# Optimization experiments

Hardware: AMD Instinct MI355X
Metric: run time of the kernel (lower is better)

## Reference

```python
import jax, jax.numpy as jnp
import numpy as np

NEG_INF = -9e15  # same masking constant as the torch module


def setup_inputs() -> dict:
    key = jax.random.key(0)
    k1, k2, k3 = jax.random.split(key, 3)
    B, S, F = 8, 2048, 128
    H, D = 4, 32  # n_heads, head_dim = out_features // n_heads
    features = jax.random.normal(k1, (B, S, F), dtype=jnp.float32)
    adj_matrix = jax.random.randint(k2, (B, S, S), 0, 2, dtype=jnp.int32)
    # Xavier-uniform-ish init for W [H, F, D]
    limit = float(np.sqrt(6.0 / (F + D)))
    W = jax.random.uniform(k3, (H, F, D), dtype=jnp.float32, minval=-limit, maxval=limit)
    return {"features": features, "adj_matrix": adj_matrix, "W": W}


def reference(features, adj_matrix, W):
    # features: [B, S, F], adj_matrix: [B, S, S] (>0 == edge), W: [H, F, D]
    D = W.shape[-1]
    Wh = jnp.einsum("bsf,hfd->bhsd", features, W)                 # [B, H, S, D]
    scores = jnp.einsum("bhsd,bhtd->bhst", Wh, Wh) / jnp.sqrt(jnp.float32(D))
    scores = jnp.where(adj_matrix[:, None, :, :] > 0, scores, NEG_INF)
    attn = jax.nn.softmax(scores, axis=-1)                         # [B, H, S, S]
    # dropout is identity at inference (training=False)
    h = jnp.einsum("bhst,bhtd->bhsd", attn, Wh)                    # [B, H, S, D]
    B, H, S, _ = h.shape
    # concat heads along feature dim, matching torch.cat(heads, dim=2)
    return jnp.transpose(h, (0, 2, 1, 3)).reshape(B, S, H * D)
```

## Files before the change

### kernel.cpp

```cpp
#include <hip/hip_runtime.h>
#include <hip/hip_bf16.h>
#include <stdint.h>


namespace {
constexpr int S = 2048;
constexpr int F = 128;
constexpr int H = 4;
constexpr int D = 32;

typedef __attribute__((ext_vector_type(4))) float f32x4;
typedef __attribute__((ext_vector_type(8))) short s16x8;
typedef __attribute__((ext_vector_type(4))) short s16x4;

__device__ __forceinline__ short f2bf(float f) {
  __hip_bfloat16 h = __float2bfloat16(f);
  short s; __builtin_memcpy(&s, &h, sizeof(s)); return s;
}
__device__ __forceinline__ float bf2f(short s) {
  __hip_bfloat16 h; __builtin_memcpy(&h, &s, sizeof(s));
  return __bfloat162float(h);
}
__device__ __forceinline__ f32x4 i4mask(int4 a) {
  f32x4 r;
  r[0] = a.x ? 1.0f : 0.0f; r[1] = a.y ? 1.0f : 0.0f;
  r[2] = a.z ? 1.0f : 0.0f; r[3] = a.w ? 1.0f : 0.0f;
  return r;
}

__global__ __launch_bounds__(256) void gat_proj(const float* __restrict__ feat,
                                                const float* __restrict__ W,
                                                short* __restrict__ Wh,
                                                short* __restrict__ WhT) {
  __shared__ __align__(16) short ftile[64][136];
  const int tid = threadIdx.x;
  const int w = tid >> 6;
  const int l = tid & 63;
  const int ln = l & 15, lg = l >> 4, g4 = (l >> 4) * 4;
  const int row0 = blockIdx.x * 64;
  const int b = row0 >> 11;
  const int sl0 = row0 & (S - 1);

#pragma unroll
  for (int i = 0; i < 4; ++i) {
    int c = i * 256 + tid;
    int r = c >> 4, c8 = (c & 15) * 8;
    const float* src = feat + (size_t)(row0 + r) * F + c8;
    float4 v0 = *(const float4*)src;
    float4 v1 = *(const float4*)(src + 4);
    s16x8 v;
    v[0]=f2bf(v0.x); v[1]=f2bf(v0.y); v[2]=f2bf(v0.z); v[3]=f2bf(v0.w);
    v[4]=f2bf(v1.x); v[5]=f2bf(v1.y); v[6]=f2bf(v1.z); v[7]=f2bf(v1.w);
    *(s16x8*)&ftile[r][c8] = v;
  }

  s16x8 bfr[4][2];
#pragma unroll
  for (int ks = 0; ks < 4; ++ks)
#pragma unroll
    for (int nt = 0; nt < 2; ++nt) {
      s16x8 v;
#pragma unroll
      for (int j = 0; j < 8; ++j)
        v[j] = f2bf(W[((size_t)w * F + ks*32 + lg*8 + j) * D + nt*16 + ln]);
      bfr[ks][nt] = v;
    }
  __syncthreads();

  const f32x4 z4 = {0.f, 0.f, 0.f, 0.f};
#pragma unroll
  for (int mt = 0; mt < 4; ++mt) {
    s16x8 a[4];
#pragma unroll
    for (int ks = 0; ks < 4; ++ks)
      a[ks] = *(const s16x8*)&ftile[mt*16 + ln][ks*32 + lg*8];
#pragma unroll
    for (int nt = 0; nt < 2; ++nt) {
      f32x4 c = z4;
#pragma unroll
      for (int ks = 0; ks < 4; ++ks)
        c = __builtin_amdgcn_mfma_f32_16x16x32_bf16(a[ks], bfr[ks][nt], c, 0, 0, 0);
      s16x4 tv;
#pragma unroll
      for (int r = 0; r < 4; ++r) {
        tv[r] = f2bf(c[r]);
        int srow = row0 + mt*16 + g4 + r;
        int s = srow & (S - 1);
        Wh[(((size_t)b * H + w) * S + s) * D + nt*16 + ln] = tv[r];
      }
      *(s16x4*)&WhT[(((size_t)b * H + w) * D + nt*16 + ln) * S + sl0 + mt*16 + g4] = tv;
    }
  }
}

__global__ __launch_bounds__(256, 3) void gat_attn(const int* __restrict__ adj,
                                                   const short* __restrict__ Wh,
                                                   const short* __restrict__ WhT,
                                                   float* __restrict__ out,
                                                   float* __restrict__ PO,
                                                   float* __restrict__ PS,
                                                   int tiles) {
  __shared__ __align__(16) float adjf[2][32][68];
  __shared__ __align__(16) short ptl[H][32][64];

  const int tid = threadIdx.x;
  const int w = tid >> 6;
  const int l = tid & 63;
  const int ln = l & 15, lg = l >> 4, g4 = (l >> 4) * 4;
  const int e3 = ln & 7;

  const int N = gridDim.x;
  const int rbid = ((int)blockIdx.x & 7) * (N >> 3) + ((int)blockIdx.x >> 3);
  const int c = rbid >> 9;
  const int g = rbid & 511;
  const int b = g >> 6;
  const int s0 = (g & 63) * 32;
  const int it0 = c * tiles;

  const short* WhBH = Wh + ((size_t)b * H + w) * S * D;
  const short* WhTBH = WhT + ((size_t)b * H + w) * D * S;
  const int* adjBase = adj + (size_t)b * S * S;
  short* pw = &ptl[w][0][0];

  const int arow = tid >> 3;
  const int ga = ((tid & 7) + arow) & 7;
  const int gb = ga + 8;
  const int* adjA = adjBase + (size_t)(s0 + arow) * S + it0*64 + ga*4;
  const int* adjBp = adjBase + (size_t)(s0 + arow) * S + it0*64 + gb*4;

  const float cs = 0.25503486f;
  s16x8 qf[2];
#pragma unroll
  for (int qt = 0; qt < 2; ++qt) {
    s16x8 v = *(const s16x8*)&WhBH[(size_t)(s0 + qt*16 + ln) * D + lg*8];
    s16x8 o;
#pragma unroll
    for (int j = 0; j < 8; ++j) o[j] = f2bf(bf2f(v[j]) * cs);
    qf[qt] = o;
  }

  const f32x4 z4 = {0.f, 0.f, 0.f, 0.f};
  f32x4 accO[2][2];
#pragma unroll
  for (int i = 0; i < 2; ++i)
#pragma unroll
    for (int j = 0; j < 2; ++j) accO[i][j] = z4;
  float psum[2] = {0.f, 0.f};

  {
    int4 a0 = *(const int4*)adjA;
    int4 a1 = *(const int4*)adjBp;
    *(f32x4*)&adjf[0][arow][ga*4] = i4mask(a0);
    *(f32x4*)&adjf[0][arow][gb*4] = i4mask(a1);
  }
  s16x8 kf[4];
  s16x8 av[2][2];
  {
    const size_t t0 = (size_t)it0 * 64;
#pragma unroll
    for (int mt = 0; mt < 4; ++mt)
      kf[mt] = *(const s16x8*)&WhBH[(t0 + mt*16 + ln) * D + lg*8];
#pragma unroll
    for (int dt = 0; dt < 2; ++dt)
#pragma unroll
      for (int kt = 0; kt < 2; ++kt)
        av[dt][kt] = *(const s16x8*)&WhTBH[(size_t)(dt*16 + ln) * S + t0 + kt*32 + lg*8];
  }
  __syncthreads();

#pragma unroll 1
  for (int i = 0; i < tiles; ++i) {
    const int cur = i & 1, nxt = cur ^ 1;
    const bool pf = (i < tiles - 1);
    const size_t t0n = (size_t)(it0 + i + 1) * 64;

    int4 a0n, a1n;
    if (pf) {
      a0n = *(const int4*)(adjA + (i + 1) * 64);
      a1n = *(const int4*)(adjBp + (i + 1) * 64);
    }

    f32x4 accS[4][2];
#pragma unroll
    for (int mt = 0; mt < 4; ++mt)
#pragma unroll
      for (int qt = 0; qt < 2; ++qt)
        accS[mt][qt] = __builtin_amdgcn_mfma_f32_16x16x32_bf16(kf[mt], qf[qt], z4, 0, 0, 0);

    if (pf) {
#pragma unroll
      for (int mt = 0; mt < 4; ++mt)
        kf[mt] = *(const s16x8*)&WhBH[(t0n + mt*16 + ln) * D + lg*8];
    }

#pragma unroll
    for (int qt = 0; qt < 2; ++qt) {
      const float* ar = &adjf[cur][qt*16 + ln][0];
#pragma unroll
      for (int mt = 0; mt < 4; ++mt) {
        f32x4 mv = *(const f32x4*)&ar[(mt*4 + lg)*4];
        f32x4 sv = accS[mt][qt];
        float p0 = __builtin_amdgcn_exp2f(sv[0]) * mv[0];
        float p1 = __builtin_amdgcn_exp2f(sv[1]) * mv[1];
        float p2 = __builtin_amdgcn_exp2f(sv[2]) * mv[2];
        float p3 = __builtin_amdgcn_exp2f(sv[3]) * mv[3];
        psum[qt] += (p0 + p1) + (p2 + p3);
        s16x4 pk;
        pk[0] = f2bf(p0); pk[1] = f2bf(p1); pk[2] = f2bf(p2); pk[3] = f2bf(p3);
        int pg = mt*2 + (lg >> 1);
        *(s16x4*)&pw[(qt*16 + ln)*64 + ((pg ^ e3) << 3) + (lg & 1)*4] = pk;
      }
    }

    s16x8 ap[2][2];
#pragma unroll
    for (int qt = 0; qt < 2; ++qt)
#pragma unroll
      for (int kt = 0; kt < 2; ++kt)
        ap[qt][kt] = *(const s16x8*)&pw[(qt*16 + ln)*64 + (((kt*4 + lg) ^ e3) << 3)];

#pragma unroll
    for (int dt = 0; dt < 2; ++dt)
#pragma unroll
      for (int qt = 0; qt < 2; ++qt)
#pragma unroll
        for (int kt = 0; kt < 2; ++kt)
          accO[dt][qt] = __builtin_amdgcn_mfma_f32_16x16x32_bf16(
              av[dt][kt], ap[qt][kt], accO[dt][qt], 0, 0, 0);

    if (pf) {
#pragma unroll
      for (int dt = 0; dt < 2; ++dt)
#pragma unroll
        for (int kt = 0; kt < 2; ++kt)
          av[dt][kt] = *(const s16x8*)&WhTBH[(size_t)(dt*16 + ln) * S + t0n + kt*32 + lg*8];
      *(f32x4*)&adjf[nxt][arow][ga*4] = i4mask(a0n);
      *(f32x4*)&adjf[nxt][arow][gb*4] = i4mask(a1n);
    }
    __syncthreads();
  }

#pragma unroll
  for (int qt = 0; qt < 2; ++qt) {
    psum[qt] += __shfl_xor(psum[qt], 16, 64);
    psum[qt] += __shfl_xor(psum[qt], 32, 64);
  }

  if (PO == nullptr) {
#pragma unroll
    for (int qt = 0; qt < 2; ++qt) {
      float inv = 1.0f / psum[qt];
#pragma unroll
      for (int dt = 0; dt < 2; ++dt) {
        f32x4 o;
#pragma unroll
        for (int r = 0; r < 4; ++r) o[r] = accO[dt][qt][r] * inv;
        *(f32x4*)&out[((size_t)b * S + s0 + qt*16 + ln) * (H * D) + w*32 + dt*16 + g4] = o;
      }
    }
  } else {
    const size_t pbase = (size_t)rbid * H + w;
    float* po = PO + pbase * 1024;
#pragma unroll
    for (int qt = 0; qt < 2; ++qt) {
#pragma unroll
      for (int dt = 0; dt < 2; ++dt)
        *(f32x4*)&po[(qt*16 + ln)*32 + dt*16 + g4] = accO[dt][qt];
      if (lg == 0) PS[pbase * 32 + qt*16 + ln] = psum[qt];
    }
  }
}

__global__ __launch_bounds__(256) void gat_reduce(const float* __restrict__ PO,
                                                  const float* __restrict__ PS,
                                                  float* __restrict__ out,
                                                  int nchunks) {
  const int f4 = blockIdx.x * 256 + threadIdx.x;
  const int d4 = f4 & 31;
  const int h = d4 >> 3;
  const int dq = d4 & 7;
  const int s_flat = f4 >> 5;
  const int b = s_flat >> 11, s = s_flat & 2047;
  const int g = b * 64 + (s >> 5), q = s & 31;

  f32x4 acc = {0.f, 0.f, 0.f, 0.f};
  float ps = 0.f;
  for (int c = 0; c < nchunks; ++c) {
    size_t pbase = ((size_t)(c * 512 + g)) * H + h;
    acc += *(const f32x4*)&PO[pbase * 1024 + q*32 + dq*4];
    ps += PS[pbase * 32 + q];
  }
  float inv = 1.0f / ps;
  f32x4 o = acc * inv;
  *(f32x4*)&out[(size_t)f4 * 4] = o;
}

}

extern "C" void kernel_launch(void* const* d_in, const int* in_sizes, int n_in,
                              void* d_out, int out_size, void* d_ws, size_t ws_size,
                              hipStream_t stream) {
  const float* feat = (const float*)d_in[0];
  const int* adj    = (const int*)d_in[1];
  const float* W    = (const float*)d_in[2];
  float* out        = (float*)d_out;

  short* Wh  = (short*)d_ws;
  short* WhT = Wh + (size_t)8 * H * S * D;
  const size_t whbytes = (size_t)2 * 8 * H * S * D * sizeof(short);
  const size_t chunkPO = (size_t)512 * H * 1024 * sizeof(float);
  const size_t chunkPS = (size_t)512 * H * 32 * sizeof(float);

  int nchunks = 1;
  if (ws_size >= whbytes + 2 * (chunkPO + chunkPS)) nchunks = 2;

  float* PO = nullptr;
  float* PS = nullptr;
  if (nchunks > 1) {
    PO = (float*)((char*)d_ws + whbytes);
    PS = (float*)((char*)d_ws + whbytes + (size_t)nchunks * chunkPO);
  }

  gat_proj<<<(8 * S) / 64, 256, 0, stream>>>(feat, W, Wh, WhT);
  gat_attn<<<512 * nchunks, 256, 0, stream>>>(adj, Wh, WhT, out, PO, PS, 32 / nchunks);
  if (nchunks > 1) gat_reduce<<<2048, 256, 0, stream>>>(PO, PS, out, nchunks);
}
```

Before: 70.19 us.

## Use bf16 bitmask masking and compute softmax row sums via ones-MFMA

Stores the adjacency mask in shared memory as 16-bit all-ones/zero masks and applies it with a bitwise AND on packed bf16 probabilities, replacing per-element float multiplies. Row sums of probabilities are accumulated by an extra MFMA against a ones vector instead of scalar adds and end-of-loop shuffles. The adjacency and K/V loads are made unconditional, clamped to the last tile, so branches leave the loop, and the S computation is interleaved per m-tile with the K prefetch. This trades VALU work for extra MFMA issue. Row sums now come from the bf16-rounded probabilities rather than the fp32 values, which slightly changes normalization.

New measurement: 76.02 us. 1.08x slower.

```diff
diff --git a/kernel.cpp b/kernel.cpp
--- a/kernel.cpp
+++ b/kernel.cpp
@@ -21,11 +21,9 @@
   __hip_bfloat16 h; __builtin_memcpy(&h, &s, sizeof(s));
   return __bfloat162float(h);
 }
-__device__ __forceinline__ f32x4 i4mask(int4 a) {
-  f32x4 r;
-  r[0] = a.x ? 1.0f : 0.0f; r[1] = a.y ? 1.0f : 0.0f;
-  r[2] = a.z ? 1.0f : 0.0f; r[3] = a.w ? 1.0f : 0.0f;
-  return r;
+__device__ __forceinline__ unsigned pkbf(float a, float b) {
+  __hip_bfloat162 h = __float22bfloat162_rn(float2{a, b});
+  unsigned u; __builtin_memcpy(&u, &h, 4); return u;
 }
 
 __global__ __launch_bounds__(256) void gat_proj(const float* __restrict__ feat,
@@ -100,7 +98,7 @@
                                                    float* __restrict__ PO,
                                                    float* __restrict__ PS,
                                                    int tiles) {
-  __shared__ __align__(16) float adjf[2][32][68];
+  __shared__ __align__(16) unsigned short maskm[2][32][72];
   __shared__ __align__(16) short ptl[H][32][64];
 
   const int tid = threadIdx.x;
@@ -108,6 +106,7 @@
   const int l = tid & 63;
   const int ln = l & 15, lg = l >> 4, g4 = (l >> 4) * 4;
   const int e3 = ln & 7;
+  const int lh = lg & 1;
 
   const int N = gridDim.x;
   const int rbid = ((int)blockIdx.x & 7) * (N >> 3) + ((int)blockIdx.x >> 3);
@@ -119,14 +118,12 @@
 
   const short* WhBH = Wh + ((size_t)b * H + w) * S * D;
   const short* WhTBH = WhT + ((size_t)b * H + w) * D * S;
-  const int* adjBase = adj + (size_t)b * S * S;
   short* pw = &ptl[w][0][0];
 
   const int arow = tid >> 3;
-  const int ga = ((tid & 7) + arow) & 7;
-  const int gb = ga + 8;
-  const int* adjA = adjBase + (size_t)(s0 + arow) * S + it0*64 + ga*4;
-  const int* adjBp = adjBase + (size_t)(s0 + arow) * S + it0*64 + gb*4;
+  const int gc = tid & 7;
+  const int* adjR = adj + (size_t)b * S * S + (size_t)(s0 + arow) * S
+                    + (size_t)it0 * 64 + gc * 8;
 
   const float cs = 0.25503486f;
   s16x8 qf[2];
@@ -139,19 +136,29 @@
     qf[qt] = o;
   }
 
+  s16x8 onesf;
+#pragma unroll
+  for (int j = 0; j < 8; ++j) onesf[j] = (short)0x3F80;
+
   const f32x4 z4 = {0.f, 0.f, 0.f, 0.f};
   f32x4 accO[2][2];
-#pragma unroll
-  for (int i = 0; i < 2; ++i)
+  f32x4 accP[2];
+#pragma unroll
+  for (int i = 0; i < 2; ++i) {
+    accP[i] = z4;
 #pragma unroll
     for (int j = 0; j < 2; ++j) accO[i][j] = z4;
-  float psum[2] = {0.f, 0.f};
+  }
 
   {
-    int4 a0 = *(const int4*)adjA;
-    int4 a1 = *(const int4*)adjBp;
-    *(f32x4*)&adjf[0][arow][ga*4] = i4mask(a0);
-    *(f32x4*)&adjf[0][arow][gb*4] = i4mask(a1);
+    int4 a0 = *(const int4*)adjR;
+    int4 a1 = *(const int4*)(adjR + 4);
+    uint4 mw;
+    mw.x = (a0.x ? 0xFFFFu : 0u) | (a0.y ? 0xFFFF0000u : 0u);
+    mw.y = (a0.z ? 0xFFFFu : 0u) | (a0.w ? 0xFFFF0000u : 0u);
+    mw.z = (a1.x ? 0xFFFFu : 0u) | (a1.y ? 0xFFFF0000u : 0u);
+    mw.w = (a1.z ? 0xFFFFu : 0u) | (a1.w ? 0xFFFF0000u : 0u);
+    *(uint4*)&maskm[0][arow][gc * 8] = mw;
   }
   s16x8 kf[4];
   s16x8 av[2][2];
@@ -170,45 +177,42 @@
 
 #pragma unroll 1
   for (int i = 0; i < tiles; ++i) {
-    const int cur = i & 1, nxt = cur ^ 1;
-    const bool pf = (i < tiles - 1);
-    const size_t t0n = (size_t)(it0 + i + 1) * 64;
-
-    int4 a0n, a1n;
-    if (pf) {
-      a0n = *(const int4*)(adjA + (i + 1) * 64);
-      a1n = *(const int4*)(adjBp + (i + 1) * 64);
-    }
-
-    f32x4 accS[4][2];
-#pragma unroll
-    for (int mt = 0; mt < 4; ++mt)
-#pragma unroll
-      for (int qt = 0; qt < 2; ++qt)
-        accS[mt][qt] = __builtin_amdgcn_mfma_f32_16x16x32_bf16(kf[mt], qf[qt], z4, 0, 0, 0);
-
-    if (pf) {
-#pragma unroll
-      for (int mt = 0; mt < 4; ++mt)
-        kf[mt] = *(const s16x8*)&WhBH[(t0n + mt*16 + ln) * D + lg*8];
-    }
-
-#pragma unroll
-    for (int qt = 0; qt < 2; ++qt) {
-      const float* ar = &adjf[cur][qt*16 + ln][0];
-#pragma unroll
-      for (int mt = 0; mt < 4; ++mt) {
-        f32x4 mv = *(const f32x4*)&ar[(mt*4 + lg)*4];
-        f32x4 sv = accS[mt][qt];
-        float p0 = __builtin_amdgcn_exp2f(sv[0]) * mv[0];
-        float p1 = __builtin_amdgcn_exp2f(sv[1]) * mv[1];
-        float p2 = __builtin_amdgcn_exp2f(sv[2]) * mv[2];
-        float p3 = __builtin_amdgcn_exp2f(sv[3]) * mv[3];
-        psum[qt] += (p0 + p1) + (p2 + p3);
-        s16x4 pk;
-        pk[0] = f2bf(p0); pk[1] = f2bf(p1); pk[2] = f2bf(p2); pk[3] = f2bf(p3);
-        int pg = mt*2 + (lg >> 1);
-        *(s16x4*)&pw[(qt*16 + ln)*64 + ((pg ^ e3) << 3) + (lg & 1)*4] = pk;
+    const int cur = i & 1;
+    const bool pf = (i + 1 < tiles);
+    const int iLd = pf ? i + 1 : i;
+    const size_t tnl = (size_t)(it0 + iLd) * 64;
+
+    int4 a0n = *(const int4*)(adjR + (size_t)iLd * 64);
+    int4 a1n = *(const int4*)(adjR + (size_t)iLd * 64 + 4);
+
+#pragma unroll
+    for (int mt = 0; mt < 4; ++mt) {
+      f32x4 sA = __builtin_amdgcn_mfma_f32_16x16x32_bf16(kf[mt], qf[0], z4, 0, 0, 0);
+      f32x4 sB = __builtin_amdgcn_mfma_f32_16x16x32_bf16(kf[mt], qf[1], z4, 0, 0, 0);
+      kf[mt] = *(const s16x8*)&WhBH[(tnl + mt*16 + ln) * D + lg*8];
+
+      const int pgo = ((mt*2 + (lg >> 1)) ^ e3) * 8 + lh * 4;
+      {
+        uint2 mm = *(const uint2*)&maskm[cur][ln][mt*16 + g4];
+        float p0 = __builtin_amdgcn_exp2f(sA[0]);
+        float p1 = __builtin_amdgcn_exp2f(sA[1]);
+        float p2 = __builtin_amdgcn_exp2f(sA[2]);
+        float p3 = __builtin_amdgcn_exp2f(sA[3]);
+        uint2 pk;
+        pk.x = pkbf(p0, p1) & mm.x;
+        pk.y = pkbf(p2, p3) & mm.y;
+        *(uint2*)&pw[ln*64 + pgo] = pk;
+      }
+      {
+        uint2 mm = *(const uint2*)&maskm[cur][16 + ln][mt*16 + g4];
+        float p0 = __builtin_amdgcn_exp2f(sB[0]);
+        float p1 = __builtin_amdgcn_exp2f(sB[1]);
+        float p2 = __builtin_amdgcn_exp2f(sB[2]);
+        float p3 = __builtin_amdgcn_exp2f(sB[3]);
+        uint2 pk;
+        pk.x = pkbf(p0, p1) & mm.x;
+        pk.y = pkbf(p2, p3) & mm.y;
+        *(uint2*)&pw[(16 + ln)*64 + pgo] = pk;
       }
     }
 
@@ -228,28 +232,34 @@
           accO[dt][qt] = __builtin_amdgcn_mfma_f32_16x16x32_bf16(
               av[dt][kt], ap[qt][kt], accO[dt][qt], 0, 0, 0);
 
+#pragma unroll
+    for (int dt = 0; dt < 2; ++dt)
+#pragma unroll
+      for (int kt = 0; kt < 2; ++kt)
+        av[dt][kt] = *(const s16x8*)&WhTBH[(size_t)(dt*16 + ln) * S + tnl + kt*32 + lg*8];
+
+#pragma unroll
+    for (int qt = 0; qt < 2; ++qt)
+#pragma unroll
+      for (int kt = 0; kt < 2; ++kt)
+        accP[qt] = __builtin_amdgcn_mfma_f32_16x16x32_bf16(
+            onesf, ap[qt][kt], accP[qt], 0, 0, 0);
+
     if (pf) {
-#pragma unroll
-      for (int dt = 0; dt < 2; ++dt)
-#pragma unroll
-        for (int kt = 0; kt < 2; ++kt)
-          av[dt][kt] = *(const s16x8*)&WhTBH[(size_t)(dt*16 + ln) * S + t0n + kt*32 + lg*8];
-      *(f32x4*)&adjf[nxt][arow][ga*4] = i4mask(a0n);
-      *(f32x4*)&adjf[nxt][arow][gb*4] = i4mask(a1n);
+      uint4 mw;
+      mw.x = (a0n.x ? 0xFFFFu : 0u) | (a0n.y ? 0xFFFF0000u : 0u);
+      mw.y = (a0n.z ? 0xFFFFu : 0u) | (a0n.w ? 0xFFFF0000u : 0u);
+      mw.z = (a1n.x ? 0xFFFFu : 0u) | (a1n.y ? 0xFFFF0000u : 0u);
+      mw.w = (a1n.z ? 0xFFFFu : 0u) | (a1n.w ? 0xFFFF0000u : 0u);
+      *(uint4*)&maskm[cur ^ 1][arow][gc * 8] = mw;
     }
     __syncthreads();
   }
 
-#pragma unroll
-  for (int qt = 0; qt < 2; ++qt) {
-    psum[qt] += __shfl_xor(psum[qt], 16, 64);
-    psum[qt] += __shfl_xor(psum[qt], 32, 64);
-  }
-
   if (PO == nullptr) {
 #pragma unroll
     for (int qt = 0; qt < 2; ++qt) {
-      float inv = 1.0f / psum[qt];
+      float inv = 1.0f / accP[qt][0];
 #pragma unroll
       for (int dt = 0; dt < 2; ++dt) {
         f32x4 o;
@@ -266,7 +276,7 @@
 #pragma unroll
       for (int dt = 0; dt < 2; ++dt)
         *(f32x4*)&po[(qt*16 + ln)*32 + dt*16 + g4] = accO[dt][qt];
-      if (lg == 0) PS[pbase * 32 + qt*16 + ln] = psum[qt];
+      if (lg == 0) PS[pbase * 32 + qt*16 + ln] = accP[qt][0];
     }
   }
 }
```
